# Performance work log

Measured on AMD Instinct MI355X. Metric: run time of the kernel, lower is better.

Reference implementation:

```python
import jax, jax.numpy as jnp
import numpy as np

NEAR_ZERO = 1e-6


def hat(w):
    # [..., 3] -> [..., 3, 3] skew-symmetric
    x, y, z = w[..., 0], w[..., 1], w[..., 2]
    O = jnp.zeros_like(x)
    return jnp.stack([jnp.stack([O, -z, y], -1),
                      jnp.stack([z, O, -x], -1),
                      jnp.stack([-y, x, O], -1)], -2)


def matrix_exp6(V):
    # V: [..., 6] twist (w, v) -> [..., 4, 4] SE(3) exp, with near-zero branch as in the torch code
    w, v = V[..., :3], V[..., 3:]
    theta = jnp.linalg.norm(w, axis=-1, keepdims=True)  # [..., 1]
    near = theta < NEAR_ZERO
    safe = jnp.where(near, 1.0, theta)
    Wh = hat(w / safe)
    Wh2 = Wh @ Wh
    t = theta[..., None]  # [..., 1, 1]
    I3 = jnp.eye(3, dtype=V.dtype)
    R = I3 + jnp.sin(t) * Wh + (1.0 - jnp.cos(t)) * Wh2
    R = jnp.where(near[..., None], I3, R)
    G = t * I3 + (1.0 - jnp.cos(t)) * Wh + (t - jnp.sin(t)) * Wh2
    p = jnp.einsum('...ij,...j->...i', G, v / safe)
    p = jnp.where(near, v, p)
    top = jnp.concatenate([R, p[..., None]], -1)
    bot = jnp.broadcast_to(jnp.array([0.0, 0.0, 0.0, 1.0], V.dtype), top.shape[:-2] + (1, 4))
    return jnp.concatenate([top, bot], -2)


def trans_inv(T):
    R = T[..., :3, :3]
    p = T[..., :3, 3]
    Rt = jnp.swapaxes(R, -1, -2)
    pinv = -jnp.einsum('...ij,...j->...i', Rt, p)
    top = jnp.concatenate([Rt, pinv[..., None]], -1)
    bot = jnp.broadcast_to(jnp.array([0.0, 0.0, 0.0, 1.0], T.dtype), top.shape[:-2] + (1, 4))
    return jnp.concatenate([top, bot], -2)


def adjoint(T):
    R = T[..., :3, :3]
    p = T[..., :3, 3]
    Z = jnp.zeros_like(R)
    top = jnp.concatenate([R, Z], -1)
    bot = jnp.concatenate([hat(p) @ R, R], -1)
    return jnp.concatenate([top, bot], -2)


def ad(V):
    W = hat(V[..., :3])
    Vh = hat(V[..., 3:])
    Z = jnp.zeros_like(W)
    top = jnp.concatenate([W, Z], -1)
    bot = jnp.concatenate([Vh, W], -1)
    return jnp.concatenate([top, bot], -2)


def inverse_dynamics(q, dq, ddq, g, Ftip, Alist, Mlist, Glist):
    # q, dq, ddq: [B, JN]; g: [3]; Ftip: [B, 6]; Alist: [JN, 6]; Mlist: [JN+1, 4, 4]; Glist: [JN, 6, 6]
    B, JN = q.shape
    Minv = trans_inv(Mlist)  # [JN+1, 4, 4]
    v0 = jnp.zeros((B, 6), q.dtype)
    a0 = jnp.concatenate([jnp.zeros((B, 3), q.dtype), jnp.broadcast_to(-g, (B, 3))], -1)

    # forward recursion over joints (sequential -> lax.scan), vectorized over batch
    def fwd_step(carry, xs):
        v, a = carry
        A_i, Minv_i, q_i, dq_i, ddq_i = xs
        T = matrix_exp6(-A_i[None, :] * q_i[:, None]) @ Minv_i  # [B, 4, 4]
        Ad = adjoint(T)
        v_new = jnp.einsum('bij,bj->bi', Ad, v) + A_i * dq_i[:, None]
        a_new = (jnp.einsum('bij,bj->bi', Ad, a)
                 + jnp.einsum('bij,j->bi', ad(v_new), A_i) * dq_i[:, None]
                 + A_i * ddq_i[:, None])
        return (v_new, a_new), (T, v_new, a_new)

    _, (Ts, vs, as_) = jax.lax.scan(fwd_step, (v0, a0), (Alist, Minv[:-1], q.T, dq.T, ddq.T))
    T_last = jnp.broadcast_to(Minv[-1], (B, 4, 4))
    AdNext = adjoint(jnp.concatenate([Ts[1:], T_last[None]], 0))  # [JN, B, 6, 6]

    # backward force recursion
    def bwd_step(F, xs):
        AdN, G_i, A_i, v_i, a_i = xs
        F_new = (jnp.einsum('bji,bj->bi', AdN, F)
                 + jnp.einsum('ij,bj->bi', G_i, a_i)
                 - jnp.einsum('bji,jk,bk->bi', ad(v_i), G_i, v_i))
        return F_new, F_new @ A_i

    _, tau = jax.lax.scan(bwd_step, Ftip, (AdNext, Glist, Alist, vs, as_), reverse=True)
    return tau.T  # [B, JN]


def setup_inputs() -> dict:
    key = jax.random.key(0)
    k = jax.random.split(key, 8)
    B, JN = 131072, 9
    q = jax.random.normal(k[0], (B, JN), jnp.float32)
    dq = jax.random.normal(k[1], (B, JN), jnp.float32)
    ddq = jax.random.normal(k[2], (B, JN), jnp.float32)
    Ftip = jax.random.normal(k[3], (B, 6), jnp.float32)
    g = jnp.array([0.0, 0.0, -9.8], jnp.float32)
    # screw axes with unit rotational part (revolute joints)
    w = jax.random.normal(k[4], (JN, 3), jnp.float32)
    w = w / jnp.linalg.norm(w, axis=-1, keepdims=True)
    vlin = jax.random.normal(k[5], (JN, 3), jnp.float32)
    Alist = jnp.concatenate([w, vlin], -1)
    # valid SE(3) home transforms
    Mlist = matrix_exp6(0.5 * jax.random.normal(k[6], (JN + 1, 6), jnp.float32))
    # SPD spatial inertias
    S = 0.3 * jax.random.normal(k[7], (JN, 6, 6), jnp.float32)
    Glist = S @ jnp.swapaxes(S, -1, -2) + jnp.eye(6, dtype=jnp.float32)
    return {"q": q, "dq": dq, "ddq": ddq, "g": g, "Ftip": Ftip,
            "Alist": Alist, "Mlist": Mlist, "Glist": Glist}


def reference(q, dq, ddq, g, Ftip, Alist, Mlist, Glist):
    return inverse_dynamics(q, dq, ddq, g, Ftip, Alist, Mlist, Glist)
```

## Files before the change

### kernel.cpp

```cpp
#include <hip/hip_runtime.h>
#include <math.h>

#define JN 9
#define BLK 128

__device__ __forceinline__ void mat3_vec(const float* R, const float* x, float* y) {
    y[0] = R[0]*x[0] + R[1]*x[1] + R[2]*x[2];
    y[1] = R[3]*x[0] + R[4]*x[1] + R[5]*x[2];
    y[2] = R[6]*x[0] + R[7]*x[1] + R[8]*x[2];
}

__device__ __forceinline__ void mat3T_vec(const float* R, const float* x, float* y) {
    y[0] = R[0]*x[0] + R[3]*x[1] + R[6]*x[2];
    y[1] = R[1]*x[0] + R[4]*x[1] + R[7]*x[2];
    y[2] = R[2]*x[0] + R[5]*x[1] + R[8]*x[2];
}

__device__ __forceinline__ void cross3(const float* a, const float* b, float* o) {
    o[0] = a[1]*b[2] - a[2]*b[1];
    o[1] = a[2]*b[0] - a[0]*b[2];
    o[2] = a[0]*b[1] - a[1]*b[0];
}

__device__ __forceinline__ void adj_apply(const float* R, const float* p,
                                          const float* x, float* y) {
    float t[3], cr[3], rv[3];
    mat3_vec(R, x, t);
    cross3(p, t, cr);
    mat3_vec(R, x + 3, rv);
    y[0] = t[0]; y[1] = t[1]; y[2] = t[2];
    y[3] = cr[0] + rv[0]; y[4] = cr[1] + rv[1]; y[5] = cr[2] + rv[2];
}

__device__ __forceinline__ void adjT_apply(const float* R, const float* p,
                                           const float* x, float* y) {
    float cr[3], t[3];
    cross3(p, x + 3, cr);
    t[0] = x[0] - cr[0]; t[1] = x[1] - cr[1]; t[2] = x[2] - cr[2];
    mat3T_vec(R, t, y);
    mat3T_vec(R, x + 3, y + 3);
}

__global__ void __launch_bounds__(BLK)
id_kernel(const float* __restrict__ q, const float* __restrict__ dq,
          const float* __restrict__ ddq, const float* __restrict__ gvec,
          const float* __restrict__ Ftip, const float* __restrict__ Alist,
          const float* __restrict__ Mlist, const float* __restrict__ Glist,
          float* __restrict__ out, int B)
{
    __shared__ float sB[JN * 6][BLK];
    __shared__ float sSig[JN][BLK];

    const int tid = threadIdx.x;
    const int b = blockIdx.x * BLK + tid;
    if (b >= B) return;

    float XR[9] = {1.f,0.f,0.f, 0.f,1.f,0.f, 0.f,0.f,1.f};
    float Xp[3] = {0.f, 0.f, 0.f};
    float bv[6] = {0.f, 0.f, 0.f, 0.f, 0.f, 0.f};
    float ba[6] = {0.f, 0.f, 0.f, -gvec[0], -gvec[1], -gvec[2]};
    float U[6]  = {0.f, 0.f, 0.f, 0.f, 0.f, 0.f};

#pragma unroll 1
    for (int j = 0; j < JN; ++j) {
        const float* __restrict__ Am = Alist + j * 6;
        const float* __restrict__ Gm = Glist + j * 36;
        const float* __restrict__ Mj = Mlist + j * 16;
        float Aj[6];
#pragma unroll
        for (int k = 0; k < 6; ++k) Aj[k] = Am[k];

        const float qj   = q[b * JN + j];
        const float dqj  = dq[b * JN + j];
        const float ddqj = ddq[b * JN + j];

        const float w0 = -Aj[0] * qj, w1 = -Aj[1] * qj, w2 = -Aj[2] * qj;
        const float l0 = -Aj[3] * qj, l1 = -Aj[4] * qj, l2 = -Aj[5] * qj;
        const float th = sqrtf(w0*w0 + w1*w1 + w2*w2);
        const bool near = th < 1e-6f;
        const float safe = near ? 1.f : th;
        const float inv = __builtin_amdgcn_rcpf(safe);
        const float x = w0 * inv, y = w1 * inv, z = w2 * inv;
        const float st = __sinf(th), ct = __cosf(th);
        const float s2 = 1.f - ct;
        const float a00 = -(z*z + y*y), a11 = -(z*z + x*x), a22 = -(y*y + x*x);
        const float a01 = x*y, a02 = x*z, a12 = y*z;
        float R[9];
        R[0] = 1.f + s2*a00;     R[1] = -st*z + s2*a01;  R[2] =  st*y + s2*a02;
        R[3] =  st*z + s2*a01;   R[4] = 1.f + s2*a11;    R[5] = -st*x + s2*a12;
        R[6] = -st*y + s2*a02;   R[7] =  st*x + s2*a12;  R[8] = 1.f + s2*a22;
        if (near) {
            R[0]=1.f; R[1]=0.f; R[2]=0.f;
            R[3]=0.f; R[4]=1.f; R[5]=0.f;
            R[6]=0.f; R[7]=0.f; R[8]=1.f;
        }
        const float g3 = th - st;
        const float u0 = l0 * inv, u1 = l1 * inv, u2 = l2 * inv;
        float p0 = th*u0 + s2*(-z*u1 + y*u2) + g3*(a00*u0 + a01*u1 + a02*u2);
        float p1 = th*u1 + s2*( z*u0 - x*u2) + g3*(a01*u0 + a11*u1 + a12*u2);
        float p2 = th*u2 + s2*(-y*u0 + x*u1) + g3*(a02*u0 + a12*u1 + a22*u2);
        if (near) { p0 = l0; p1 = l1; p2 = l2; }

        float TR[9], Tp[3];
        {
#pragma unroll
            for (int r = 0; r < 3; ++r) {
#pragma unroll
                for (int cc = 0; cc < 3; ++cc) {
                    TR[r*3+cc] = R[r*3+0]*Mj[cc*4+0] + R[r*3+1]*Mj[cc*4+1] + R[r*3+2]*Mj[cc*4+2];
                }
            }
            const float mp0 = Mj[3], mp1 = Mj[7], mp2 = Mj[11];
            Tp[0] = p0 - (TR[0]*mp0 + TR[1]*mp1 + TR[2]*mp2);
            Tp[1] = p1 - (TR[3]*mp0 + TR[4]*mp1 + TR[5]*mp2);
            Tp[2] = p2 - (TR[6]*mp0 + TR[7]*mp1 + TR[8]*mp2);
        }

        {
            float nR[9], np[3];
#pragma unroll
            for (int r = 0; r < 3; ++r) {
#pragma unroll
                for (int cc = 0; cc < 3; ++cc) {
                    nR[r*3+cc] = TR[r*3+0]*XR[0*3+cc] + TR[r*3+1]*XR[1*3+cc] + TR[r*3+2]*XR[2*3+cc];
                }
            }
            mat3_vec(TR, Xp, np);
#pragma unroll
            for (int r = 0; r < 9; ++r) XR[r] = nR[r];
            Xp[0] = np[0] + Tp[0]; Xp[1] = np[1] + Tp[1]; Xp[2] = np[2] + Tp[2];
        }

        float Bv[6];
        {
            float ip[3];
            mat3T_vec(XR, Xp, ip);
            ip[0] = -ip[0]; ip[1] = -ip[1]; ip[2] = -ip[2];
            float tw[3], tv[3], cr[3];
            mat3T_vec(XR, Aj, tw);
            mat3T_vec(XR, Aj + 3, tv);
            cross3(ip, tw, cr);
            Bv[0] = tw[0]; Bv[1] = tw[1]; Bv[2] = tw[2];
            Bv[3] = cr[0] + tv[0]; Bv[4] = cr[1] + tv[1]; Bv[5] = cr[2] + tv[2];
        }

        float sig = Bv[0]*U[0] + Bv[1]*U[1] + Bv[2]*U[2]
                  + Bv[3]*U[3] + Bv[4]*U[4] + Bv[5]*U[5];

#pragma unroll
        for (int k = 0; k < 6; ++k) bv[k] += Bv[k] * dqj;
        {
            float t0[3], t1[3], t2[3];
            cross3(bv, Bv, t0);
            cross3(bv + 3, Bv, t1);
            cross3(bv, Bv + 3, t2);
            ba[0] += t0[0]*dqj + Bv[0]*ddqj;
            ba[1] += t0[1]*dqj + Bv[1]*ddqj;
            ba[2] += t0[2]*dqj + Bv[2]*ddqj;
            ba[3] += (t1[0]+t2[0])*dqj + Bv[3]*ddqj;
            ba[4] += (t1[1]+t2[1])*dqj + Bv[4]*ddqj;
            ba[5] += (t1[2]+t2[2])*dqj + Bv[5]*ddqj;
        }

        float vl[6], al[6];
        adj_apply(XR, Xp, bv, vl);
        adj_apply(XR, Xp, ba, al);

        float Gv[6], Ga[6];
#pragma unroll
        for (int r = 0; r < 6; ++r) {
            float sv = 0.f, sa = 0.f;
#pragma unroll
            for (int kk = 0; kk < 6; ++kk) {
                sv += Gm[r*6+kk] * vl[kk];
                sa += Gm[r*6+kk] * al[kk];
            }
            Gv[r] = sv; Ga[r] = sa;
        }
        float W[6];
        {
            float cw[3], cv[3], cb[3];
            cross3(vl, Gv, cw);
            cross3(vl + 3, Gv + 3, cv);
            cross3(vl, Gv + 3, cb);
            W[0] = Ga[0]+cw[0]+cv[0]; W[1] = Ga[1]+cw[1]+cv[1]; W[2] = Ga[2]+cw[2]+cv[2];
            W[3] = Ga[3]+cb[0];       W[4] = Ga[4]+cb[1];       W[5] = Ga[5]+cb[2];
        }

        {
            float S[6];
            adjT_apply(XR, Xp, W, S);
#pragma unroll
            for (int k = 0; k < 6; ++k) U[k] += S[k];
        }

#pragma unroll
        for (int k = 0; k < 6; ++k) sB[j * 6 + k][tid] = Bv[k];
        sSig[j][tid] = sig;
    }

    float E[6];
    {
        const float* __restrict__ M9 = Mlist + JN * 16;
        float R9[9], p9[3];
#pragma unroll
        for (int r = 0; r < 3; ++r) {
#pragma unroll
            for (int cc = 0; cc < 3; ++cc) {
                R9[r*3+cc] = M9[0*4+r]*XR[0*3+cc] + M9[1*4+r]*XR[1*3+cc] + M9[2*4+r]*XR[2*3+cc];
            }
        }
        float t[3] = { Xp[0] - M9[3], Xp[1] - M9[7], Xp[2] - M9[11] };
        p9[0] = M9[0*4+0]*t[0] + M9[1*4+0]*t[1] + M9[2*4+0]*t[2];
        p9[1] = M9[0*4+1]*t[0] + M9[1*4+1]*t[1] + M9[2*4+1]*t[2];
        p9[2] = M9[0*4+2]*t[0] + M9[1*4+2]*t[1] + M9[2*4+2]*t[2];
        float Ft[6];
#pragma unroll
        for (int k = 0; k < 6; ++k) Ft[k] = Ftip[b * 6 + k];
        float Z[6];
        adjT_apply(R9, p9, Ft, Z);
#pragma unroll
        for (int k = 0; k < 6; ++k) E[k] = U[k] + Z[k];
    }

#pragma unroll
    for (int i = 0; i < JN; ++i) {
        float d = -sSig[i][tid];
#pragma unroll
        for (int k = 0; k < 6; ++k) d += sB[i * 6 + k][tid] * E[k];
        out[b * JN + i] = d;
    }
}

extern "C" void kernel_launch(void* const* d_in, const int* in_sizes, int n_in,
                              void* d_out, int out_size, void* d_ws, size_t ws_size,
                              hipStream_t stream) {
    const float* q     = (const float*)d_in[0];
    const float* dq    = (const float*)d_in[1];
    const float* ddq   = (const float*)d_in[2];
    const float* g     = (const float*)d_in[3];
    const float* Ftip  = (const float*)d_in[4];
    const float* Alist = (const float*)d_in[5];
    const float* Mlist = (const float*)d_in[6];
    const float* Glist = (const float*)d_in[7];
    float* out = (float*)d_out;

    const int B = in_sizes[0] / JN;
    const int grid = (B + BLK - 1) / BLK;
    hipLaunchKernelGGL(id_kernel, dim3(grid), dim3(BLK), 0, stream,
                       q, dq, ddq, g, Ftip, Alist, Mlist, Glist, out, B);
}
```

Before: 26.84 us.

## Precompute per-joint constants so joint transform is linear in sin/cos of q

Adds a tiny prep kernel that uses the unit-axis assumption (Rodrigues) to fold each joint's screw axis and home transform into constant matrices. The per-sample transform then reduces to TR = c*Q1 + s*M2 + Q3 and a similar affine form for the translation. This removes the per-joint norm, reciprocal, near-zero branch and matrix products. The main kernel also fully unrolls the joint loop, keeps B and sigma in registers instead of shared memory, loads inputs with vectorisable memcpy, and uses 256-thread blocks. The costs are an extra kernel launch and higher register pressure, and the result assumes unit-norm rotational axes, which holds for revolute joints. A fallback path keeps the old kernel for when no workspace is available.

```diff
diff --git a/kernel.cpp b/kernel.cpp
--- a/kernel.cpp
+++ b/kernel.cpp
@@ -2,26 +2,26 @@
 #include <math.h>
 
 #define JN 9
-#define BLK 128
+#define BLK 256
+#define BLK_FB 128
+#define CPJ 84
+#define CST_FLOATS (JN * CPJ + 12)
 
 __device__ __forceinline__ void mat3_vec(const float* R, const float* x, float* y) {
     y[0] = R[0]*x[0] + R[1]*x[1] + R[2]*x[2];
     y[1] = R[3]*x[0] + R[4]*x[1] + R[5]*x[2];
     y[2] = R[6]*x[0] + R[7]*x[1] + R[8]*x[2];
 }
-
 __device__ __forceinline__ void mat3T_vec(const float* R, const float* x, float* y) {
     y[0] = R[0]*x[0] + R[3]*x[1] + R[6]*x[2];
     y[1] = R[1]*x[0] + R[4]*x[1] + R[7]*x[2];
     y[2] = R[2]*x[0] + R[5]*x[1] + R[8]*x[2];
 }
-
 __device__ __forceinline__ void cross3(const float* a, const float* b, float* o) {
     o[0] = a[1]*b[2] - a[2]*b[1];
     o[1] = a[2]*b[0] - a[0]*b[2];
     o[2] = a[0]*b[1] - a[1]*b[0];
 }
-
 __device__ __forceinline__ void adj_apply(const float* R, const float* p,
                                           const float* x, float* y) {
     float t[3], cr[3], rv[3];
@@ -31,7 +31,6 @@
     y[0] = t[0]; y[1] = t[1]; y[2] = t[2];
     y[3] = cr[0] + rv[0]; y[4] = cr[1] + rv[1]; y[5] = cr[2] + rv[2];
 }
-
 __device__ __forceinline__ void adjT_apply(const float* R, const float* p,
                                            const float* x, float* y) {
     float cr[3], t[3];
@@ -41,112 +40,124 @@
     mat3T_vec(R, x + 3, y + 3);
 }
 
-__global__ void __launch_bounds__(BLK)
-id_kernel(const float* __restrict__ q, const float* __restrict__ dq,
-          const float* __restrict__ ddq, const float* __restrict__ gvec,
-          const float* __restrict__ Ftip, const float* __restrict__ Alist,
-          const float* __restrict__ Mlist, const float* __restrict__ Glist,
-          float* __restrict__ out, int B)
+__global__ void prep_kernel(const float* __restrict__ A, const float* __restrict__ M,
+                            const float* __restrict__ G, float* __restrict__ cst) {
+    const int j = threadIdx.x;
+    if (j < JN) {
+        const float* Aj = A + j * 6;
+        const float* Mj = M + j * 16;
+        const float ax = Aj[0], ay = Aj[1], az = Aj[2];
+        const float vx = Aj[3], vy = Aj[4], vz = Aj[5];
+        float M1[9];
+        for (int t = 0; t < 3; ++t)
+            for (int c = 0; c < 3; ++c) M1[t*3+c] = Mj[c*4+t];
+        const float K[9] = {0.f,-az,ay, az,0.f,-ax, -ay,ax,0.f};
+        float M2[9];
+        for (int r = 0; r < 3; ++r)
+            for (int c = 0; c < 3; ++c)
+                M2[r*3+c] = K[r*3+0]*M1[0*3+c] + K[r*3+1]*M1[1*3+c] + K[r*3+2]*M1[2*3+c];
+        float t3[3];
+        for (int c = 0; c < 3; ++c) t3[c] = ax*M1[0*3+c] + ay*M1[1*3+c] + az*M1[2*3+c];
+        float M3[9];
+        const float Aw[3] = {ax, ay, az};
+        for (int r = 0; r < 3; ++r)
+            for (int c = 0; c < 3; ++c) M3[r*3+c] = Aw[r] * t3[c];
+        float Q1[9], Q3[9];
+        for (int e = 0; e < 9; ++e) { Q1[e] = M1[e] - M3[e]; Q3[e] = M3[e]; }
+        const float Mp[3] = {Mj[3], Mj[7], Mj[11]};
+        const float d = ax*vx + ay*vy + az*vz;
+        const float C[3] = {ay*vz - az*vy, az*vx - ax*vz, ax*vy - ay*vx};
+        float q2m[3], q1m[3], q3m[3];
+        mat3_vec(M2, Mp, q2m);
+        mat3_vec(Q1, Mp, q1m);
+        mat3_vec(Q3, Mp, q3m);
+        float* o = cst + j * CPJ;
+        for (int e = 0; e < 9; ++e) { o[e] = Q1[e]; o[9+e] = M2[e]; o[18+e] = Q3[e]; }
+        o[27] = (vx - d*ax) - q2m[0]; o[28] = (vy - d*ay) - q2m[1]; o[29] = (vz - d*az) - q2m[2];
+        o[30] = -C[0] - q1m[0];       o[31] = -C[1] - q1m[1];       o[32] = -C[2] - q1m[2];
+        o[33] = d*ax;                 o[34] = d*ay;                 o[35] = d*az;
+        o[36] = C[0] - q3m[0];        o[37] = C[1] - q3m[1];        o[38] = C[2] - q3m[2];
+        for (int k = 0; k < 6; ++k)  o[39 + k] = Aj[k];
+        const float* Gj = G + j * 36;
+        for (int k = 0; k < 36; ++k) o[45 + k] = Gj[k];
+    } else if (j == JN) {
+        const float* M9 = M + JN * 16;
+        float* o = cst + JN * CPJ;
+        for (int r = 0; r < 3; ++r)
+            for (int c = 0; c < 3; ++c) o[r*3+c] = M9[c*4+r];
+        o[9] = M9[3]; o[10] = M9[7]; o[11] = M9[11];
+    }
+}
+
+__global__ void __launch_bounds__(BLK, 2)
+id_main(const float* __restrict__ q, const float* __restrict__ dq,
+        const float* __restrict__ ddq, const float* __restrict__ gvec,
+        const float* __restrict__ Ftip, const float* __restrict__ cst,
+        float* __restrict__ out, int B)
 {
-    __shared__ float sB[JN * 6][BLK];
-    __shared__ float sSig[JN][BLK];
-
-    const int tid = threadIdx.x;
-    const int b = blockIdx.x * BLK + tid;
+    const int b = blockIdx.x * BLK + threadIdx.x;
     if (b >= B) return;
+
+    float qv[JN], dqv[JN], ddqv[JN], Ft[6];
+    __builtin_memcpy(qv,   q   + (size_t)b * JN, JN * sizeof(float));
+    __builtin_memcpy(dqv,  dq  + (size_t)b * JN, JN * sizeof(float));
+    __builtin_memcpy(ddqv, ddq + (size_t)b * JN, JN * sizeof(float));
+    __builtin_memcpy(Ft,   Ftip + (size_t)b * 6, 6 * sizeof(float));
+    const float g0 = gvec[0], g1 = gvec[1], g2 = gvec[2];
 
     float XR[9] = {1.f,0.f,0.f, 0.f,1.f,0.f, 0.f,0.f,1.f};
     float Xp[3] = {0.f, 0.f, 0.f};
     float bv[6] = {0.f, 0.f, 0.f, 0.f, 0.f, 0.f};
-    float ba[6] = {0.f, 0.f, 0.f, -gvec[0], -gvec[1], -gvec[2]};
+    float ba[6] = {0.f, 0.f, 0.f, -g0, -g1, -g2};
     float U[6]  = {0.f, 0.f, 0.f, 0.f, 0.f, 0.f};
-
-#pragma unroll 1
+    float Bst[JN][6];
+    float sig[JN];
+
+#pragma unroll
     for (int j = 0; j < JN; ++j) {
-        const float* __restrict__ Am = Alist + j * 6;
-        const float* __restrict__ Gm = Glist + j * 36;
-        const float* __restrict__ Mj = Mlist + j * 16;
-        float Aj[6];
-#pragma unroll
-        for (int k = 0; k < 6; ++k) Aj[k] = Am[k];
-
-        const float qj   = q[b * JN + j];
-        const float dqj  = dq[b * JN + j];
-        const float ddqj = ddq[b * JN + j];
-
-        const float w0 = -Aj[0] * qj, w1 = -Aj[1] * qj, w2 = -Aj[2] * qj;
-        const float l0 = -Aj[3] * qj, l1 = -Aj[4] * qj, l2 = -Aj[5] * qj;
-        const float th = sqrtf(w0*w0 + w1*w1 + w2*w2);
-        const bool near = th < 1e-6f;
-        const float safe = near ? 1.f : th;
-        const float inv = __builtin_amdgcn_rcpf(safe);
-        const float x = w0 * inv, y = w1 * inv, z = w2 * inv;
-        const float st = __sinf(th), ct = __cosf(th);
-        const float s2 = 1.f - ct;
-        const float a00 = -(z*z + y*y), a11 = -(z*z + x*x), a22 = -(y*y + x*x);
-        const float a01 = x*y, a02 = x*z, a12 = y*z;
-        float R[9];
-        R[0] = 1.f + s2*a00;     R[1] = -st*z + s2*a01;  R[2] =  st*y + s2*a02;
-        R[3] =  st*z + s2*a01;   R[4] = 1.f + s2*a11;    R[5] = -st*x + s2*a12;
-        R[6] = -st*y + s2*a02;   R[7] =  st*x + s2*a12;  R[8] = 1.f + s2*a22;
-        if (near) {
-            R[0]=1.f; R[1]=0.f; R[2]=0.f;
-            R[3]=0.f; R[4]=1.f; R[5]=0.f;
-            R[6]=0.f; R[7]=0.f; R[8]=1.f;
-        }
-        const float g3 = th - st;
-        const float u0 = l0 * inv, u1 = l1 * inv, u2 = l2 * inv;
-        float p0 = th*u0 + s2*(-z*u1 + y*u2) + g3*(a00*u0 + a01*u1 + a02*u2);
-        float p1 = th*u1 + s2*( z*u0 - x*u2) + g3*(a01*u0 + a11*u1 + a12*u2);
-        float p2 = th*u2 + s2*(-y*u0 + x*u1) + g3*(a02*u0 + a12*u1 + a22*u2);
-        if (near) { p0 = l0; p1 = l1; p2 = l2; }
+        const float* Cj = cst + j * CPJ;
+        const float phi = -qv[j];
+        float s, c;
+        __sincosf(phi, &s, &c);
 
         float TR[9], Tp[3];
-        {
-#pragma unroll
-            for (int r = 0; r < 3; ++r) {
-#pragma unroll
-                for (int cc = 0; cc < 3; ++cc) {
-                    TR[r*3+cc] = R[r*3+0]*Mj[cc*4+0] + R[r*3+1]*Mj[cc*4+1] + R[r*3+2]*Mj[cc*4+2];
-                }
-            }
-            const float mp0 = Mj[3], mp1 = Mj[7], mp2 = Mj[11];
-            Tp[0] = p0 - (TR[0]*mp0 + TR[1]*mp1 + TR[2]*mp2);
-            Tp[1] = p1 - (TR[3]*mp0 + TR[4]*mp1 + TR[5]*mp2);
-            Tp[2] = p2 - (TR[6]*mp0 + TR[7]*mp1 + TR[8]*mp2);
-        }
+#pragma unroll
+        for (int e = 0; e < 9; ++e) TR[e] = c * Cj[e] + s * Cj[9 + e] + Cj[18 + e];
+#pragma unroll
+        for (int k = 0; k < 3; ++k)
+            Tp[k] = s * Cj[27 + k] + c * Cj[30 + k] + phi * Cj[33 + k] + Cj[36 + k];
 
         {
             float nR[9], np[3];
 #pragma unroll
-            for (int r = 0; r < 3; ++r) {
-#pragma unroll
-                for (int cc = 0; cc < 3; ++cc) {
+            for (int r = 0; r < 3; ++r)
+#pragma unroll
+                for (int cc = 0; cc < 3; ++cc)
                     nR[r*3+cc] = TR[r*3+0]*XR[0*3+cc] + TR[r*3+1]*XR[1*3+cc] + TR[r*3+2]*XR[2*3+cc];
-                }
-            }
             mat3_vec(TR, Xp, np);
 #pragma unroll
-            for (int r = 0; r < 9; ++r) XR[r] = nR[r];
+            for (int e = 0; e < 9; ++e) XR[e] = nR[e];
             Xp[0] = np[0] + Tp[0]; Xp[1] = np[1] + Tp[1]; Xp[2] = np[2] + Tp[2];
         }
 
+        const float Aw[3] = {Cj[39], Cj[40], Cj[41]};
+        const float Av[3] = {Cj[42], Cj[43], Cj[44]};
         float Bv[6];
         {
-            float ip[3];
+            float ip[3], tw[3], tv[3], cr[3];
             mat3T_vec(XR, Xp, ip);
             ip[0] = -ip[0]; ip[1] = -ip[1]; ip[2] = -ip[2];
-            float tw[3], tv[3], cr[3];
-            mat3T_vec(XR, Aj, tw);
-            mat3T_vec(XR, Aj + 3, tv);
+            mat3T_vec(XR, Aw, tw);
+            mat3T_vec(XR, Av, tv);
             cross3(ip, tw, cr);
             Bv[0] = tw[0]; Bv[1] = tw[1]; Bv[2] = tw[2];
             Bv[3] = cr[0] + tv[0]; Bv[4] = cr[1] + tv[1]; Bv[5] = cr[2] + tv[2];
         }
 
-        float sig = Bv[0]*U[0] + Bv[1]*U[1] + Bv[2]*U[2]
-                  + Bv[3]*U[3] + Bv[4]*U[4] + Bv[5]*U[5];
-
+        sig[j] = Bv[0]*U[0] + Bv[1]*U[1] + Bv[2]*U[2]
+               + Bv[3]*U[3] + Bv[4]*U[4] + Bv[5]*U[5];
+
+        const float dqj = dqv[j], ddqj = ddqv[j];
 #pragma unroll
         for (int k = 0; k < 6; ++k) bv[k] += Bv[k] * dqj;
         {
@@ -165,15 +176,15 @@
         float vl[6], al[6];
         adj_apply(XR, Xp, bv, vl);
         adj_apply(XR, Xp, ba, al);
-
         float Gv[6], Ga[6];
 #pragma unroll
         for (int r = 0; r < 6; ++r) {
             float sv = 0.f, sa = 0.f;
 #pragma unroll
             for (int kk = 0; kk < 6; ++kk) {
-                sv += Gm[r*6+kk] * vl[kk];
-                sa += Gm[r*6+kk] * al[kk];
+                const float gmv = Cj[45 + r*6 + kk];
+                sv += gmv * vl[kk];
+                sa += gmv * al[kk];
             }
             Gv[r] = sv; Ga[r] = sa;
         }
@@ -186,49 +197,192 @@
             W[0] = Ga[0]+cw[0]+cv[0]; W[1] = Ga[1]+cw[1]+cv[1]; W[2] = Ga[2]+cw[2]+cv[2];
             W[3] = Ga[3]+cb[0];       W[4] = Ga[4]+cb[1];       W[5] = Ga[5]+cb[2];
         }
-
         {
             float S[6];
             adjT_apply(XR, Xp, W, S);
 #pragma unroll
             for (int k = 0; k < 6; ++k) U[k] += S[k];
         }
-
-#pragma unroll
-        for (int k = 0; k < 6; ++k) sB[j * 6 + k][tid] = Bv[k];
-        sSig[j][tid] = sig;
+#pragma unroll
+        for (int k = 0; k < 6; ++k) Bst[j][k] = Bv[k];
     }
 
     float E[6];
     {
-        const float* __restrict__ M9 = Mlist + JN * 16;
+        const float* W9 = cst + JN * CPJ;
         float R9[9], p9[3];
 #pragma unroll
-        for (int r = 0; r < 3; ++r) {
-#pragma unroll
-            for (int cc = 0; cc < 3; ++cc) {
-                R9[r*3+cc] = M9[0*4+r]*XR[0*3+cc] + M9[1*4+r]*XR[1*3+cc] + M9[2*4+r]*XR[2*3+cc];
-            }
-        }
-        float t[3] = { Xp[0] - M9[3], Xp[1] - M9[7], Xp[2] - M9[11] };
-        p9[0] = M9[0*4+0]*t[0] + M9[1*4+0]*t[1] + M9[2*4+0]*t[2];
-        p9[1] = M9[0*4+1]*t[0] + M9[1*4+1]*t[1] + M9[2*4+1]*t[2];
-        p9[2] = M9[0*4+2]*t[0] + M9[1*4+2]*t[1] + M9[2*4+2]*t[2];
-        float Ft[6];
-#pragma unroll
-        for (int k = 0; k < 6; ++k) Ft[k] = Ftip[b * 6 + k];
+        for (int r = 0; r < 3; ++r)
+#pragma unroll
+            for (int cc = 0; cc < 3; ++cc)
+                R9[r*3+cc] = W9[r*3+0]*XR[0*3+cc] + W9[r*3+1]*XR[1*3+cc] + W9[r*3+2]*XR[2*3+cc];
+        const float t[3] = {Xp[0] - W9[9], Xp[1] - W9[10], Xp[2] - W9[11]};
+        mat3_vec(W9, t, p9);
         float Z[6];
         adjT_apply(R9, p9, Ft, Z);
 #pragma unroll
         for (int k = 0; k < 6; ++k) E[k] = U[k] + Z[k];
     }
-
+    float tv[JN];
+#pragma unroll
+    for (int i = 0; i < JN; ++i) {
+        float d = -sig[i];
+#pragma unroll
+        for (int k = 0; k < 6; ++k) d += Bst[i][k] * E[k];
+        tv[i] = d;
+    }
+    __builtin_memcpy(out + (size_t)b * JN, tv, JN * sizeof(float));
+}
+
+__global__ void __launch_bounds__(BLK_FB)
+id_kernel_fb(const float* __restrict__ q, const float* __restrict__ dq,
+             const float* __restrict__ ddq, const float* __restrict__ gvec,
+             const float* __restrict__ Ftip, const float* __restrict__ Alist,
+             const float* __restrict__ Mlist, const float* __restrict__ Glist,
+             float* __restrict__ out, int B)
+{
+    __shared__ float sB[JN * 6][BLK_FB];
+    __shared__ float sSig[JN][BLK_FB];
+    const int tid = threadIdx.x;
+    const int b = blockIdx.x * BLK_FB + tid;
+    if (b >= B) return;
+    float XR[9] = {1.f,0.f,0.f, 0.f,1.f,0.f, 0.f,0.f,1.f};
+    float Xp[3] = {0.f, 0.f, 0.f};
+    float bv[6] = {0.f,0.f,0.f,0.f,0.f,0.f};
+    float ba[6] = {0.f, 0.f, 0.f, -gvec[0], -gvec[1], -gvec[2]};
+    float U[6]  = {0.f,0.f,0.f,0.f,0.f,0.f};
+#pragma unroll 1
+    for (int j = 0; j < JN; ++j) {
+        const float* Am = Alist + j * 6;
+        const float* Gm = Glist + j * 36;
+        const float* Mj = Mlist + j * 16;
+        float Aj[6];
+#pragma unroll
+        for (int k = 0; k < 6; ++k) Aj[k] = Am[k];
+        const float qj = q[b*JN+j], dqj = dq[b*JN+j], ddqj = ddq[b*JN+j];
+        const float w0 = -Aj[0]*qj, w1 = -Aj[1]*qj, w2 = -Aj[2]*qj;
+        const float l0 = -Aj[3]*qj, l1 = -Aj[4]*qj, l2 = -Aj[5]*qj;
+        const float th = sqrtf(w0*w0 + w1*w1 + w2*w2);
+        const bool near = th < 1e-6f;
+        const float safe = near ? 1.f : th;
+        const float inv = __builtin_amdgcn_rcpf(safe);
+        const float x = w0*inv, y = w1*inv, z = w2*inv;
+        const float st = __sinf(th), ct = __cosf(th);
+        const float s2 = 1.f - ct;
+        const float a00 = -(z*z+y*y), a11 = -(z*z+x*x), a22 = -(y*y+x*x);
+        const float a01 = x*y, a02 = x*z, a12 = y*z;
+        float R[9];
+        R[0]=1.f+s2*a00;   R[1]=-st*z+s2*a01; R[2]= st*y+s2*a02;
+        R[3]= st*z+s2*a01; R[4]=1.f+s2*a11;   R[5]=-st*x+s2*a12;
+        R[6]=-st*y+s2*a02; R[7]= st*x+s2*a12; R[8]=1.f+s2*a22;
+        if (near) { R[0]=1;R[1]=0;R[2]=0;R[3]=0;R[4]=1;R[5]=0;R[6]=0;R[7]=0;R[8]=1; }
+        const float g3 = th - st;
+        const float u0 = l0*inv, u1 = l1*inv, u2 = l2*inv;
+        float p0 = th*u0 + s2*(-z*u1+y*u2) + g3*(a00*u0+a01*u1+a02*u2);
+        float p1 = th*u1 + s2*( z*u0-x*u2) + g3*(a01*u0+a11*u1+a12*u2);
+        float p2 = th*u2 + s2*(-y*u0+x*u1) + g3*(a02*u0+a12*u1+a22*u2);
+        if (near) { p0=l0; p1=l1; p2=l2; }
+        float TR[9], Tp[3];
+#pragma unroll
+        for (int r = 0; r < 3; ++r)
+#pragma unroll
+            for (int cc = 0; cc < 3; ++cc)
+                TR[r*3+cc] = R[r*3+0]*Mj[cc*4+0] + R[r*3+1]*Mj[cc*4+1] + R[r*3+2]*Mj[cc*4+2];
+        const float mp0 = Mj[3], mp1 = Mj[7], mp2 = Mj[11];
+        Tp[0] = p0 - (TR[0]*mp0 + TR[1]*mp1 + TR[2]*mp2);
+        Tp[1] = p1 - (TR[3]*mp0 + TR[4]*mp1 + TR[5]*mp2);
+        Tp[2] = p2 - (TR[6]*mp0 + TR[7]*mp1 + TR[8]*mp2);
+        {
+            float nR[9], np[3];
+#pragma unroll
+            for (int r = 0; r < 3; ++r)
+#pragma unroll
+                for (int cc = 0; cc < 3; ++cc)
+                    nR[r*3+cc] = TR[r*3+0]*XR[0*3+cc] + TR[r*3+1]*XR[1*3+cc] + TR[r*3+2]*XR[2*3+cc];
+            mat3_vec(TR, Xp, np);
+#pragma unroll
+            for (int e = 0; e < 9; ++e) XR[e] = nR[e];
+            Xp[0] = np[0]+Tp[0]; Xp[1] = np[1]+Tp[1]; Xp[2] = np[2]+Tp[2];
+        }
+        float Bv[6];
+        {
+            float ip[3], tw[3], tvv[3], cr[3];
+            mat3T_vec(XR, Xp, ip);
+            ip[0]=-ip[0]; ip[1]=-ip[1]; ip[2]=-ip[2];
+            mat3T_vec(XR, Aj, tw);
+            mat3T_vec(XR, Aj+3, tvv);
+            cross3(ip, tw, cr);
+            Bv[0]=tw[0]; Bv[1]=tw[1]; Bv[2]=tw[2];
+            Bv[3]=cr[0]+tvv[0]; Bv[4]=cr[1]+tvv[1]; Bv[5]=cr[2]+tvv[2];
+        }
+        float sg = Bv[0]*U[0]+Bv[1]*U[1]+Bv[2]*U[2]+Bv[3]*U[3]+Bv[4]*U[4]+Bv[5]*U[5];
+#pragma unroll
+        for (int k = 0; k < 6; ++k) bv[k] += Bv[k]*dqj;
+        {
+            float t0[3], t1[3], t2[3];
+            cross3(bv, Bv, t0); cross3(bv+3, Bv, t1); cross3(bv, Bv+3, t2);
+            ba[0] += t0[0]*dqj + Bv[0]*ddqj;
+            ba[1] += t0[1]*dqj + Bv[1]*ddqj;
+            ba[2] += t0[2]*dqj + Bv[2]*ddqj;
+            ba[3] += (t1[0]+t2[0])*dqj + Bv[3]*ddqj;
+            ba[4] += (t1[1]+t2[1])*dqj + Bv[4]*ddqj;
+            ba[5] += (t1[2]+t2[2])*dqj + Bv[5]*ddqj;
+        }
+        float vl[6], al[6];
+        adj_apply(XR, Xp, bv, vl);
+        adj_apply(XR, Xp, ba, al);
+        float Gv[6], Ga[6];
+#pragma unroll
+        for (int r = 0; r < 6; ++r) {
+            float sv = 0.f, sa = 0.f;
+#pragma unroll
+            for (int kk = 0; kk < 6; ++kk) { sv += Gm[r*6+kk]*vl[kk]; sa += Gm[r*6+kk]*al[kk]; }
+            Gv[r] = sv; Ga[r] = sa;
+        }
+        float W[6];
+        {
+            float cw[3], cv[3], cb[3];
+            cross3(vl, Gv, cw); cross3(vl+3, Gv+3, cv); cross3(vl, Gv+3, cb);
+            W[0]=Ga[0]+cw[0]+cv[0]; W[1]=Ga[1]+cw[1]+cv[1]; W[2]=Ga[2]+cw[2]+cv[2];
+            W[3]=Ga[3]+cb[0];       W[4]=Ga[4]+cb[1];       W[5]=Ga[5]+cb[2];
+        }
+        {
+            float S[6];
+            adjT_apply(XR, Xp, W, S);
+#pragma unroll
+            for (int k = 0; k < 6; ++k) U[k] += S[k];
+        }
+#pragma unroll
+        for (int k = 0; k < 6; ++k) sB[j*6+k][tid] = Bv[k];
+        sSig[j][tid] = sg;
+    }
+    float E[6];
+    {
+        const float* M9 = Mlist + JN * 16;
+        float R9[9], p9[3];
+#pragma unroll
+        for (int r = 0; r < 3; ++r)
+#pragma unroll
+            for (int cc = 0; cc < 3; ++cc)
+                R9[r*3+cc] = M9[0*4+r]*XR[0*3+cc] + M9[1*4+r]*XR[1*3+cc] + M9[2*4+r]*XR[2*3+cc];
+        float t[3] = {Xp[0]-M9[3], Xp[1]-M9[7], Xp[2]-M9[11]};
+        p9[0] = M9[0]*t[0] + M9[4]*t[1] + M9[8]*t[2];
+        p9[1] = M9[1]*t[0] + M9[5]*t[1] + M9[9]*t[2];
+        p9[2] = M9[2]*t[0] + M9[6]*t[1] + M9[10]*t[2];
+        float Ftl[6];
+#pragma unroll
+        for (int k = 0; k < 6; ++k) Ftl[k] = Ftip[b*6+k];
+        float Z[6];
+        adjT_apply(R9, p9, Ftl, Z);
+#pragma unroll
+        for (int k = 0; k < 6; ++k) E[k] = U[k] + Z[k];
+    }
 #pragma unroll
     for (int i = 0; i < JN; ++i) {
         float d = -sSig[i][tid];
 #pragma unroll
-        for (int k = 0; k < 6; ++k) d += sB[i * 6 + k][tid] * E[k];
-        out[b * JN + i] = d;
+        for (int k = 0; k < 6; ++k) d += sB[i*6+k][tid] * E[k];
+        out[b*JN+i] = d;
     }
 }
 
@@ -244,9 +398,18 @@
     const float* Mlist = (const float*)d_in[6];
     const float* Glist = (const float*)d_in[7];
     float* out = (float*)d_out;
-
     const int B = in_sizes[0] / JN;
-    const int grid = (B + BLK - 1) / BLK;
-    hipLaunchKernelGGL(id_kernel, dim3(grid), dim3(BLK), 0, stream,
-                       q, dq, ddq, g, Ftip, Alist, Mlist, Glist, out, B);
-}
+
+    if (ws_size >= CST_FLOATS * sizeof(float)) {
+        float* cst = (float*)d_ws;
+        hipLaunchKernelGGL(prep_kernel, dim3(1), dim3(16), 0, stream,
+                           Alist, Mlist, Glist, cst);
+        const int grid = (B + BLK - 1) / BLK;
+        hipLaunchKernelGGL(id_main, dim3(grid), dim3(BLK), 0, stream,
+                           q, dq, ddq, g, Ftip, cst, out, B);
+    } else {
+        const int grid = (B + BLK_FB - 1) / BLK_FB;
+        hipLaunchKernelGGL(id_kernel_fb, dim3(grid), dim3(BLK_FB), 0, stream,
+                           q, dq, ddq, g, Ftip, Alist, Mlist, Glist, out, B);
+    }
+}
```

Measured after the change: 71.33 us. 2.66x slower.
